# Performance work log

Measured on AMD Instinct MI355X. Metric: run time of the kernel, lower is better.

The kernel has to match this reference:

```python
import jax, jax.numpy as jnp
import numpy as np

SEQ_LEN = 4_194_304  # number of tokens
INPUT_BITS = 16      # bits per token, MSB first


def setup_inputs() -> dict:
    key = jax.random.key(0)
    # bits in {0,1}; float32 carrier (values exact, matches uint8 bit semantics)
    tokens = jax.random.randint(key, (SEQ_LEN, INPUT_BITS), 0, 2).astype(jnp.float32)
    return {"tokens": tokens}


def reference(tokens):
    # tokens: [seq_len, input_bits], MSB first, entries in {0,1}
    bits = tokens.shape[1]
    # _bits_to_int: val = val*2 + b  ==  dot with [2^(bits-1), ..., 2, 1]
    pow2 = jnp.exp2(jnp.arange(bits - 1, -1, -1, dtype=jnp.float32))  # [bits]
    values = tokens @ pow2  # [seq_len], exact for bits <= 24
    # stable ascending sort == Python list.sort on (value, original_index)
    order = jnp.argsort(values, stable=True)  # [seq_len]
    return tokens[order]  # gather rows by rank
```

## Files before the change

### kernel.cpp

```cpp
#include <hip/hip_runtime.h>
#include <stdint.h>

static constexpr uint32_t SEQN = 4194304u;
static constexpr uint32_t BINS = 65536u;
static constexpr uint32_t QWORDS = BINS / 4u;
static constexpr uint32_t NBLK = 256u;
static constexpr uint32_t NTHR = 1024u;
static constexpr uint32_t ROWS_PER_BLK = SEQN / NBLK;

__global__ __launch_bounds__(NTHR) void k_hist_lds(const float4* __restrict__ in4,
                                                   uint32_t* __restrict__ partial,
                                                   uint32_t* __restrict__ blkTot) {
  __shared__ __align__(16) uint32_t h[QWORDS];
  uint32_t tid = threadIdx.x, blk = blockIdx.x;
  if (blk == 0u && tid < 64u) blkTot[tid] = 0u;
  uint4* hv = (uint4*)h;
  for (uint32_t i = tid; i < QWORDS / 4u; i += NTHR) hv[i] = make_uint4(0u, 0u, 0u, 0u);
  __syncthreads();
  uint32_t q = tid & 3u;
  uint32_t shift = 12u - (q << 2);
  bool leader = (q == 0u);
  const float4* base = in4 + (size_t)blk * (ROWS_PER_BLK * 4u);
#pragma unroll
  for (uint32_t b = 0; b < 8u; ++b) {
    float4 v[8];
#pragma unroll
    for (uint32_t u = 0; u < 8u; ++u)
      v[u] = base[(size_t)(b * 8u + u) * NTHR + tid];
#pragma unroll
    for (uint32_t u = 0; u < 8u; ++u) {
      float nf = ((v[u].x * 2.0f + v[u].y) * 2.0f + v[u].z) * 2.0f + v[u].w;
      uint32_t part = ((uint32_t)nf) << shift;
      uint32_t s1 = part + (uint32_t)__builtin_amdgcn_mov_dpp((int)part, 0xB1, 0xF, 0xF, true);
      uint32_t key = s1 + (uint32_t)__builtin_amdgcn_mov_dpp((int)s1, 0x4E, 0xF, 0xF, true);
      if (leader) atomicAdd(&h[key >> 2], 1u << ((key & 3u) << 3));
    }
  }
  __syncthreads();
  uint4* dst = (uint4*)(partial + (size_t)blk * QWORDS);
  for (uint32_t i = tid; i < QWORDS / 4u; i += NTHR) dst[i] = hv[i];
}

__global__ __launch_bounds__(256) void k_reduceD(const uint32_t* __restrict__ partial,
                                                 uint32_t* __restrict__ hist,
                                                 uint32_t* __restrict__ blkTot) {
  __shared__ uint2 acc[4][64];
  uint32_t tid = threadIdx.x, b = blockIdx.x;
  uint32_t wl = tid & 63u, g = tid >> 6;
  uint32_t w = b * 64u + wl;
  uint32_t e = 0u, o = 0u;
  uint32_t p0 = g * 64u;
#pragma unroll 8
  for (uint32_t p = p0; p < p0 + 64u; ++p) {
    uint32_t v = partial[(size_t)p * QWORDS + w];
    e += v & 0x00FF00FFu;
    o += (v >> 8) & 0x00FF00FFu;
  }
  acc[g][wl] = make_uint2(e, o);
  __syncthreads();
  if (g == 0u) {
    uint2 a1 = acc[1][wl], a2 = acc[2][wl], a3 = acc[3][wl];
    e += a1.x + a2.x + a3.x;
    o += a1.y + a2.y + a3.y;
    uint32_t c0 = e & 0xFFFFu, c2 = e >> 16, c1 = o & 0xFFFFu, c3 = o >> 16;
    ((uint4*)hist)[w] = make_uint4(c0, c1, c2, c3);
    uint32_t ssum = c0 + c1 + c2 + c3;
    for (int d = 1; d < 64; d <<= 1) ssum += __shfl_xor(ssum, d, 64);
    if (wl == 0u) atomicAdd(&blkTot[b >> 2], ssum);
  }
}

__global__ __launch_bounds__(256) void k_zero(uint32_t* __restrict__ hist,
                                              uint32_t* __restrict__ blkTot) {
  uint32_t i = blockIdx.x * 256u + threadIdx.x;
  if (i < BINS) hist[i] = 0u;
  if (i < 64u) blkTot[i] = 0u;
}

__global__ __launch_bounds__(256) void k_hist(const float4* __restrict__ in4,
                                              uint32_t* __restrict__ hist) {
  uint32_t r = blockIdx.x * 256u + threadIdx.x;
  if (r >= SEQN) return;
  uint32_t key = 0u;
#pragma unroll
  for (uint32_t qq = 0; qq < 4u; ++qq) {
    float4 v = in4[(size_t)r * 4u + qq];
    uint32_t nib = ((uint32_t)v.x << 3) | ((uint32_t)v.y << 2) |
                   ((uint32_t)v.z << 1) | (uint32_t)v.w;
    key = (key << 4) | nib;
  }
  atomicAdd(&hist[key], 1u);
}

__global__ __launch_bounds__(256) void k_scan1(const uint32_t* __restrict__ hist,
                                               uint32_t* __restrict__ blkTot) {
  uint32_t tid = threadIdx.x, blk = blockIdx.x;
  uint32_t b0 = blk * 1024u + tid * 4u;
  uint32_t s = hist[b0] + hist[b0 + 1] + hist[b0 + 2] + hist[b0 + 3];
  for (int d = 1; d < 64; d <<= 1) s += __shfl_xor(s, d, 64);
  __shared__ uint32_t wt[4];
  if ((tid & 63u) == 0u) wt[tid >> 6] = s;
  __syncthreads();
  if (tid == 0u) blkTot[blk] = wt[0] + wt[1] + wt[2] + wt[3];
}

__global__ __launch_bounds__(256) void k_scanB(const uint32_t* __restrict__ hist,
                                               const uint32_t* __restrict__ blkTot,
                                               uint32_t* __restrict__ offs) {
  __shared__ uint32_t s_base;
  __shared__ uint32_t wt[4];
  uint32_t tid = threadIdx.x, blk = blockIdx.x;
  if (tid < 64u) {
    uint32_t v = blkTot[tid];
    uint32_t incl = v;
    for (int d = 1; d < 64; d <<= 1) {
      uint32_t n = __shfl_up(incl, d, 64);
      if (tid >= (uint32_t)d) incl += n;
    }
    if (tid == blk) s_base = incl - v;
  }
  __syncthreads();
  uint32_t lane = tid & 63u, wid = tid >> 6;
  uint32_t b0 = blk * 1024u + tid * 4u;
  uint4 c = ((const uint4*)hist)[b0 >> 2];
  uint32_t s = c.x + c.y + c.z + c.w;
  uint32_t incl = s;
  for (int d = 1; d < 64; d <<= 1) {
    uint32_t n = __shfl_up(incl, d, 64);
    if (lane >= (uint32_t)d) incl += n;
  }
  if (lane == 63u) wt[wid] = incl;
  __syncthreads();
  uint32_t wbase = 0u;
  for (uint32_t w = 0; w < wid; ++w) wbase += wt[w];
  uint32_t base = s_base + wbase + (incl - s);
  ((uint4*)offs)[b0 >> 2] = make_uint4(base, base + c.x, base + c.x + c.y,
                                       base + c.x + c.y + c.z);
}

__global__ __launch_bounds__(256) void k_write_range(const uint32_t* __restrict__ offs,
                                                     float4* __restrict__ out4) {
  __shared__ uint32_t s_off[33];
  uint32_t tid = threadIdx.x, blk = blockIdx.x;
  if (tid < 33u) {
    uint32_t k = blk * 32u + tid;
    s_off[tid] = (k < BINS) ? offs[k] : SEQN;
  }
  __syncthreads();
  uint32_t lane = tid & 63u, wid = tid >> 6;
  uint32_t kbase = blk * 32u + wid * 8u;
  uint32_t q0 = s_off[wid * 8u] * 4u;
  uint32_t q8 = s_off[wid * 8u + 8u] * 4u;
  uint32_t b1 = s_off[wid * 8u + 1u] * 4u, b2 = s_off[wid * 8u + 2u] * 4u;
  uint32_t b3 = s_off[wid * 8u + 3u] * 4u, b4 = s_off[wid * 8u + 4u] * 4u;
  uint32_t b5 = s_off[wid * 8u + 5u] * 4u, b6 = s_off[wid * 8u + 6u] * 4u;
  uint32_t b7 = s_off[wid * 8u + 7u] * 4u;
  uint32_t sh = 12u - ((lane & 3u) << 2);
  for (uint32_t g = q0 + lane; g < q8; g += 64u) {
    uint32_t kl = (uint32_t)(g >= b1) + (uint32_t)(g >= b2) + (uint32_t)(g >= b3) +
                  (uint32_t)(g >= b4) + (uint32_t)(g >= b5) + (uint32_t)(g >= b6) +
                  (uint32_t)(g >= b7);
    uint32_t key = kbase + kl;
    uint32_t nib = (key >> sh) & 15u;
    float4 pat;
    pat.x = (float)((nib >> 3) & 1u);
    pat.y = (float)((nib >> 2) & 1u);
    pat.z = (float)((nib >> 1) & 1u);
    pat.w = (float)(nib & 1u);
    out4[g] = pat;
  }
}

extern "C" void kernel_launch(void* const* d_in, const int* in_sizes, int n_in,
                              void* d_out, int out_size, void* d_ws, size_t ws_size,
                              hipStream_t stream) {
  const float4* in4 = (const float4*)d_in[0];
  float4* out4 = (float4*)d_out;
  uint32_t* hist = (uint32_t*)d_ws;
  uint32_t* offs = hist + BINS;
  uint32_t* blkTot = offs + BINS;
  uint32_t* partial = blkTot + 1024u;

  size_t need = ((size_t)2 * BINS + 1024u + (size_t)NBLK * QWORDS) * 4u;
  if (ws_size >= need) {
    k_hist_lds<<<NBLK, NTHR, 0, stream>>>(in4, partial, blkTot);
    k_reduceD<<<256, 256, 0, stream>>>(partial, hist, blkTot);
  } else {
    k_zero<<<BINS / 256, 256, 0, stream>>>(hist, blkTot);
    k_hist<<<SEQN / 256, 256, 0, stream>>>(in4, hist);
    k_scan1<<<64, 256, 0, stream>>>(hist, blkTot);
  }
  k_scanB<<<64, 256, 0, stream>>>(hist, blkTot, offs);
  k_write_range<<<BINS / 32, 256, 0, stream>>>(offs, out4);
}
```

Measured before the change: 134.0 us.

## Fuse partial-histogram reduction with scan and compute group sums in histogram kernel

The histogram kernel now also computes per-block sums for each of 64 bin groups and writes them to a small groupSum buffer, replacing the global atomic block totals. The separate reduce and scan kernels are merged into one 64-block, 1024-thread kernel. Each block reduces its 1024 bins across all partials, derives its base offset from the groupSum table, and writes the offsets directly. This drops one kernel launch and the hist round trip through global memory. In exchange, the reduction uses fewer, larger blocks (64 instead of 256), which lowers parallelism on the memory-bound partial reduction.

```diff
diff --git a/kernel.cpp b/kernel.cpp
--- a/kernel.cpp
+++ b/kernel.cpp
@@ -10,12 +10,13 @@
 
 __global__ __launch_bounds__(NTHR) void k_hist_lds(const float4* __restrict__ in4,
                                                    uint32_t* __restrict__ partial,
-                                                   uint32_t* __restrict__ blkTot) {
+                                                   uint32_t* __restrict__ groupSum) {
   __shared__ __align__(16) uint32_t h[QWORDS];
-  uint32_t tid = threadIdx.x, blk = blockIdx.x;
-  if (blk == 0u && tid < 64u) blkTot[tid] = 0u;
+  __shared__ uint32_t gsum[64];
+  uint32_t tid = threadIdx.x, blk = blockIdx.x;
   uint4* hv = (uint4*)h;
   for (uint32_t i = tid; i < QWORDS / 4u; i += NTHR) hv[i] = make_uint4(0u, 0u, 0u, 0u);
+  if (tid < 64u) gsum[tid] = 0u;
   __syncthreads();
   uint32_t q = tid & 3u;
   uint32_t shift = 12u - (q << 2);
@@ -39,34 +40,76 @@
   __syncthreads();
   uint4* dst = (uint4*)(partial + (size_t)blk * QWORDS);
   for (uint32_t i = tid; i < QWORDS / 4u; i += NTHR) dst[i] = hv[i];
-}
-
-__global__ __launch_bounds__(256) void k_reduceD(const uint32_t* __restrict__ partial,
-                                                 uint32_t* __restrict__ hist,
-                                                 uint32_t* __restrict__ blkTot) {
-  __shared__ uint2 acc[4][64];
-  uint32_t tid = threadIdx.x, b = blockIdx.x;
-  uint32_t wl = tid & 63u, g = tid >> 6;
-  uint32_t w = b * 64u + wl;
+  uint32_t wsum = 0u;
+#pragma unroll
+  for (uint32_t i = 0; i < 16u; ++i) {
+    uint32_t v = h[tid * 16u + i];
+    wsum += (v & 0x00FF00FFu) + ((v >> 8) & 0x00FF00FFu);
+  }
+  wsum = (wsum & 0xFFFFu) + (wsum >> 16);
+  atomicAdd(&gsum[tid >> 4], wsum);
+  __syncthreads();
+  if (tid < 64u) groupSum[blk * 64u + tid] = gsum[tid];
+}
+
+__global__ __launch_bounds__(NTHR) void k_redscan(const uint32_t* __restrict__ partial,
+                                                  const uint32_t* __restrict__ groupSum,
+                                                  uint32_t* __restrict__ offs) {
+  __shared__ uint2 acc[4][256];
+  __shared__ uint32_t gpart[16][64];
+  __shared__ uint32_t s_base;
+  __shared__ uint32_t wt[4];
+  uint32_t tid = threadIdx.x, g = blockIdx.x;
+  uint32_t col = tid & 63u, chunk = tid >> 6;
+  uint32_t gs = 0u;
+#pragma unroll
+  for (uint32_t r = 0; r < 16u; ++r) gs += groupSum[(chunk * 16u + r) * 64u + col];
+  gpart[chunk][col] = gs;
+  uint32_t wl = tid & 255u, grp = tid >> 8;
+  uint32_t w = g * 256u + wl;
   uint32_t e = 0u, o = 0u;
-  uint32_t p0 = g * 64u;
+  uint32_t p0 = grp * 64u;
 #pragma unroll 8
   for (uint32_t p = p0; p < p0 + 64u; ++p) {
     uint32_t v = partial[(size_t)p * QWORDS + w];
     e += v & 0x00FF00FFu;
     o += (v >> 8) & 0x00FF00FFu;
   }
-  acc[g][wl] = make_uint2(e, o);
-  __syncthreads();
-  if (g == 0u) {
-    uint2 a1 = acc[1][wl], a2 = acc[2][wl], a3 = acc[3][wl];
-    e += a1.x + a2.x + a3.x;
-    o += a1.y + a2.y + a3.y;
-    uint32_t c0 = e & 0xFFFFu, c2 = e >> 16, c1 = o & 0xFFFFu, c3 = o >> 16;
-    ((uint4*)hist)[w] = make_uint4(c0, c1, c2, c3);
-    uint32_t ssum = c0 + c1 + c2 + c3;
-    for (int d = 1; d < 64; d <<= 1) ssum += __shfl_xor(ssum, d, 64);
-    if (wl == 0u) atomicAdd(&blkTot[b >> 2], ssum);
+  acc[grp][wl] = make_uint2(e, o);
+  __syncthreads();
+  uint32_t c0 = 0, c1 = 0, c2 = 0, c3 = 0, ssum = 0, incl = 0;
+  uint32_t lane = tid & 63u, wid = tid >> 6;
+  if (tid < 64u) {
+    uint32_t t = 0u;
+#pragma unroll
+    for (uint32_t i = 0; i < 16u; ++i) t += gpart[i][tid];
+    uint32_t ti = t;
+    for (int d = 1; d < 64; d <<= 1) {
+      uint32_t n = __shfl_up(ti, d, 64);
+      if (tid >= (uint32_t)d) ti += n;
+    }
+    if (tid == g) s_base = ti - t;
+  }
+  if (tid < 256u) {
+    uint2 a0 = acc[0][wl], a1 = acc[1][wl], a2 = acc[2][wl], a3 = acc[3][wl];
+    uint32_t E = a0.x + a1.x + a2.x + a3.x;
+    uint32_t O = a0.y + a1.y + a2.y + a3.y;
+    c0 = E & 0xFFFFu; c2 = E >> 16; c1 = O & 0xFFFFu; c3 = O >> 16;
+    ssum = c0 + c1 + c2 + c3;
+    incl = ssum;
+    for (int d = 1; d < 64; d <<= 1) {
+      uint32_t n = __shfl_up(incl, d, 64);
+      if (lane >= (uint32_t)d) incl += n;
+    }
+    if (lane == 63u) wt[wid] = incl;
+  }
+  __syncthreads();
+  if (tid < 256u) {
+    uint32_t wbase = 0u;
+    for (uint32_t ww = 0; ww < wid; ++ww) wbase += wt[ww];
+    uint32_t base = s_base + wbase + (incl - ssum);
+    ((uint4*)offs)[w] = make_uint4(base, base + c0, base + c0 + c1,
+                                   base + c0 + c1 + c2);
   }
 }
 
@@ -180,16 +223,17 @@
   uint32_t* offs = hist + BINS;
   uint32_t* blkTot = offs + BINS;
   uint32_t* partial = blkTot + 1024u;
-
-  size_t need = ((size_t)2 * BINS + 1024u + (size_t)NBLK * QWORDS) * 4u;
+  uint32_t* groupSum = partial + (size_t)NBLK * QWORDS;
+
+  size_t need = ((size_t)2 * BINS + 1024u + (size_t)NBLK * QWORDS + NBLK * 64u) * 4u;
   if (ws_size >= need) {
-    k_hist_lds<<<NBLK, NTHR, 0, stream>>>(in4, partial, blkTot);
-    k_reduceD<<<256, 256, 0, stream>>>(partial, hist, blkTot);
+    k_hist_lds<<<NBLK, NTHR, 0, stream>>>(in4, partial, groupSum);
+    k_redscan<<<64, NTHR, 0, stream>>>(partial, groupSum, offs);
   } else {
     k_zero<<<BINS / 256, 256, 0, stream>>>(hist, blkTot);
     k_hist<<<SEQN / 256, 256, 0, stream>>>(in4, hist);
     k_scan1<<<64, 256, 0, stream>>>(hist, blkTot);
-  }
-  k_scanB<<<64, 256, 0, stream>>>(hist, blkTot, offs);
+    k_scanB<<<64, 256, 0, stream>>>(hist, blkTot, offs);
+  }
   k_write_range<<<BINS / 32, 256, 0, stream>>>(offs, out4);
 }
```

After: 132.8 us (median of 2 runs). About the same (-0.9%).

## Fuse histogram reduction with prefix scan using per-block chunk sums

Applied to the files above, without the earlier changes.

The histogram kernel now also writes per-block sums for each 256-bin chunk. A new reduce kernel uses these to compute each chunk's global base with a local scan, then reduces the partial histograms and writes exclusive offsets directly. This removes the separate scan kernel launch and the atomic block-total pass. In exchange, every reduce block redundantly reads the full 256x256 chunk-sum table.

```diff
diff --git a/kernel.cpp b/kernel.cpp
--- a/kernel.cpp
+++ b/kernel.cpp
@@ -10,12 +10,13 @@
 
 __global__ __launch_bounds__(NTHR) void k_hist_lds(const float4* __restrict__ in4,
                                                    uint32_t* __restrict__ partial,
-                                                   uint32_t* __restrict__ blkTot) {
+                                                   uint32_t* __restrict__ chunkSum) {
   __shared__ __align__(16) uint32_t h[QWORDS];
-  uint32_t tid = threadIdx.x, blk = blockIdx.x;
-  if (blk == 0u && tid < 64u) blkTot[tid] = 0u;
+  __shared__ uint32_t gsum[256];
+  uint32_t tid = threadIdx.x, blk = blockIdx.x;
   uint4* hv = (uint4*)h;
   for (uint32_t i = tid; i < QWORDS / 4u; i += NTHR) hv[i] = make_uint4(0u, 0u, 0u, 0u);
+  if (tid < 256u) gsum[tid] = 0u;
   __syncthreads();
   uint32_t q = tid & 3u;
   uint32_t shift = 12u - (q << 2);
@@ -39,13 +40,46 @@
   __syncthreads();
   uint4* dst = (uint4*)(partial + (size_t)blk * QWORDS);
   for (uint32_t i = tid; i < QWORDS / 4u; i += NTHR) dst[i] = hv[i];
-}
-
-__global__ __launch_bounds__(256) void k_reduceD(const uint32_t* __restrict__ partial,
-                                                 uint32_t* __restrict__ hist,
-                                                 uint32_t* __restrict__ blkTot) {
+  uint32_t wsum = 0u;
+#pragma unroll
+  for (uint32_t i = 0; i < 16u; ++i) {
+    uint32_t v = h[tid * 16u + i];
+    wsum += (v & 0x00FF00FFu) + ((v >> 8) & 0x00FF00FFu);
+  }
+  wsum = (wsum & 0xFFFFu) + (wsum >> 16);
+  atomicAdd(&gsum[tid >> 2], wsum);
+  __syncthreads();
+  if (tid < 256u) chunkSum[blk * 256u + tid] = gsum[tid];
+}
+
+__global__ __launch_bounds__(256) void k_redscan2(const uint32_t* __restrict__ partial,
+                                                  const uint32_t* __restrict__ chunkSum,
+                                                  uint32_t* __restrict__ offs) {
+  __shared__ uint32_t tot[256];
+  __shared__ uint32_t sc[256];
   __shared__ uint2 acc[4][64];
+  __shared__ uint32_t wt[4];
   uint32_t tid = threadIdx.x, b = blockIdx.x;
+  uint32_t t = 0u;
+#pragma unroll 8
+  for (uint32_t p = 0; p < 256u; ++p) t += chunkSum[p * 256u + tid];
+  tot[tid] = t;
+  __syncthreads();
+  {
+    uint32_t lane = tid & 63u, wid = tid >> 6;
+    uint32_t v = tot[tid], incl = v;
+    for (int d = 1; d < 64; d <<= 1) {
+      uint32_t n = __shfl_up(incl, d, 64);
+      if (lane >= (uint32_t)d) incl += n;
+    }
+    if (lane == 63u) wt[wid] = incl;
+    __syncthreads();
+    uint32_t wbase = 0u;
+    for (uint32_t w = 0; w < wid; ++w) wbase += wt[w];
+    sc[tid] = wbase + incl - v;
+  }
+  __syncthreads();
+  uint32_t base0 = sc[b];
   uint32_t wl = tid & 63u, g = tid >> 6;
   uint32_t w = b * 64u + wl;
   uint32_t e = 0u, o = 0u;
@@ -58,15 +92,20 @@
   }
   acc[g][wl] = make_uint2(e, o);
   __syncthreads();
-  if (g == 0u) {
-    uint2 a1 = acc[1][wl], a2 = acc[2][wl], a3 = acc[3][wl];
-    e += a1.x + a2.x + a3.x;
-    o += a1.y + a2.y + a3.y;
-    uint32_t c0 = e & 0xFFFFu, c2 = e >> 16, c1 = o & 0xFFFFu, c3 = o >> 16;
-    ((uint4*)hist)[w] = make_uint4(c0, c1, c2, c3);
+  if (tid < 64u) {
+    uint2 a0 = acc[0][tid], a1 = acc[1][tid], a2 = acc[2][tid], a3 = acc[3][tid];
+    uint32_t E = a0.x + a1.x + a2.x + a3.x;
+    uint32_t O = a0.y + a1.y + a2.y + a3.y;
+    uint32_t c0 = E & 0xFFFFu, c2 = E >> 16, c1 = O & 0xFFFFu, c3 = O >> 16;
     uint32_t ssum = c0 + c1 + c2 + c3;
-    for (int d = 1; d < 64; d <<= 1) ssum += __shfl_xor(ssum, d, 64);
-    if (wl == 0u) atomicAdd(&blkTot[b >> 2], ssum);
+    uint32_t incl = ssum;
+    for (int d = 1; d < 64; d <<= 1) {
+      uint32_t n = __shfl_up(incl, d, 64);
+      if (tid >= (uint32_t)d) incl += n;
+    }
+    uint32_t base = base0 + (incl - ssum);
+    ((uint4*)offs)[w] = make_uint4(base, base + c0, base + c0 + c1,
+                                   base + c0 + c1 + c2);
   }
 }
 
@@ -180,16 +219,17 @@
   uint32_t* offs = hist + BINS;
   uint32_t* blkTot = offs + BINS;
   uint32_t* partial = blkTot + 1024u;
-
-  size_t need = ((size_t)2 * BINS + 1024u + (size_t)NBLK * QWORDS) * 4u;
+  uint32_t* chunkSum = partial + (size_t)NBLK * QWORDS;
+
+  size_t need = ((size_t)2 * BINS + 1024u + (size_t)NBLK * QWORDS + NBLK * 256u) * 4u;
   if (ws_size >= need) {
-    k_hist_lds<<<NBLK, NTHR, 0, stream>>>(in4, partial, blkTot);
-    k_reduceD<<<256, 256, 0, stream>>>(partial, hist, blkTot);
+    k_hist_lds<<<NBLK, NTHR, 0, stream>>>(in4, partial, chunkSum);
+    k_redscan2<<<256, 256, 0, stream>>>(partial, chunkSum, offs);
   } else {
     k_zero<<<BINS / 256, 256, 0, stream>>>(hist, blkTot);
     k_hist<<<SEQN / 256, 256, 0, stream>>>(in4, hist);
     k_scan1<<<64, 256, 0, stream>>>(hist, blkTot);
-  }
-  k_scanB<<<64, 256, 0, stream>>>(hist, blkTot, offs);
+    k_scanB<<<64, 256, 0, stream>>>(hist, blkTot, offs);
+  }
   k_write_range<<<BINS / 32, 256, 0, stream>>>(offs, out4);
 }
```

New measurement: 138.1 us. 3.1% more time.
